# Performance work log

Measured on AMD Instinct MI355X. Metric: run time of the kernel, lower is better.

## Reference

```python
import jax, jax.numpy as jnp
import numpy as np
from jax import lax

B, CIN, COUT, WDIM, K, H, W_ = 8, 512, 512, 512, 3, 64, 64

def setup_inputs() -> dict:
    key = jax.random.key(0)
    ks = jax.random.split(key, 7)
    x = jax.random.normal(ks[0], (B, CIN, H, W_), dtype=jnp.float32)
    w = jax.random.normal(ks[1], (B, WDIM), dtype=jnp.float32)
    noise = jax.random.normal(ks[2], (B, COUT, H, W_), dtype=jnp.float32)
    # params (kaiming-ish scale for weight; demodulation normalizes anyway)
    weight = jax.random.normal(ks[3], (1, COUT, CIN, K, K), dtype=jnp.float32) * 0.05
    affine_w = jax.random.normal(ks[4], (CIN, WDIM), dtype=jnp.float32) * (1.0 / np.sqrt(WDIM))
    affine_b = jnp.zeros((CIN,), dtype=jnp.float32)
    bias = jnp.zeros((COUT,), dtype=jnp.float32)
    return {"x": x, "w": w, "noise": noise, "weight": weight,
            "affine_w": affine_w, "affine_b": affine_b, "bias": bias}

def reference(x, w, noise, weight, affine_w, affine_b, bias):
    b, cin, h, ww = x.shape
    cout, k = weight.shape[1], weight.shape[3]
    # style: affine(w) + 1
    s = jnp.einsum('bd,cd->bc', w, affine_w) + affine_b          # [B, Cin]
    s = s[:, None, :, None, None] + 1.0                           # [B,1,Cin,1,1]
    w_mod = weight * s                                            # [B,Cout,Cin,k,k]
    d = lax.rsqrt(jnp.sum(w_mod * w_mod, axis=(2, 3, 4), keepdims=True) + 1e-8)
    w_mod = w_mod * d
    # grouped conv: groups = B
    x_ = x.reshape(1, b * cin, h, ww)
    w_ = w_mod.reshape(b * cout, cin, k, k)
    pad = k // 2
    y = lax.conv_general_dilated(
        x_, w_, window_strides=(1, 1), padding=[(pad, pad), (pad, pad)],
        feature_group_count=b,
        dimension_numbers=('NCHW', 'OIHW', 'NCHW'))
    y = y.reshape(b, cout, h, ww)
    y = y + noise + bias[None, :, None, None]
    return jnp.where(y >= 0, y, 0.2 * y)
```

## Files before the change

### kernel.cpp

```cpp
#include <hip/hip_runtime.h>
#include <hip/hip_bf16.h>


#define CIN   512
#define COUT  512
#define KDIM  4608
#define HWPIX 4096

typedef __attribute__((ext_vector_type(8))) __bf16 bf16x8;
typedef __attribute__((ext_vector_type(4))) float  f32x4;

__device__ __forceinline__ unsigned short f2bf(float f){
  union { float f; unsigned int u; } v; v.f = f;
  unsigned int u = v.u;
  u += 0x7fffu + ((u >> 16) & 1u);
  return (unsigned short)(u >> 16);
}

#define GLDS16(g, l) __builtin_amdgcn_global_load_lds(                      \
    (const __attribute__((address_space(1))) unsigned int*)(g),             \
    (__attribute__((address_space(3))) unsigned int*)(l), 16, 0, 0)

__global__ void style_k(const float* __restrict__ w, const float* __restrict__ aw,
                        const float* __restrict__ ab, float* __restrict__ styles){
  int wid = threadIdx.x >> 6, lane = threadIdx.x & 63;
  int gid = blockIdx.x * 4 + wid;
  int b = gid >> 9, c = gid & 511;
  const float* wb = w + b * 512;
  const float* ar = aw + c * 512;
  float sum = 0.f;
  for (int j = lane; j < 512; j += 64) sum += wb[j] * ar[j];
  for (int off = 32; off; off >>= 1) sum += __shfl_down(sum, off, 64);
  if (lane == 0) styles[gid] = sum + ab[c] + 1.0f;
}

__global__ void modw_k(const float* __restrict__ weight, const float* __restrict__ styles,
                       unsigned short* __restrict__ wmod){
  int o = blockIdx.x, b = blockIdx.y;
  int t = threadIdx.x;
  const float* wrow = weight + (size_t)o * KDIM;
  const float* st   = styles + b * 512;
  __shared__ unsigned short sw[9 * 520];
  __shared__ float red[4];
  float vals[18];
  float part = 0.f;
#pragma unroll
  for (int it = 0; it < 18; ++it){
    int idx = it * 256 + t;
    int i = idx / 9;
    float v = wrow[idx] * st[i];
    vals[it] = v;
    part += v * v;
  }
  int wid = t >> 6, lane = t & 63;
  for (int off = 32; off; off >>= 1) part += __shfl_down(part, off, 64);
  if (lane == 0) red[wid] = part;
  __syncthreads();
  float d = rsqrtf(red[0] + red[1] + red[2] + red[3] + 1e-8f);
#pragma unroll
  for (int it = 0; it < 18; ++it){
    int idx = it * 256 + t;
    int i = idx / 9;
    int tap = idx - i * 9;
    sw[tap * 520 + i] = f2bf(vals[it] * d);
  }
  __syncthreads();
  unsigned int* orow32 = (unsigned int*)(wmod + ((size_t)(b * 512 + o)) * KDIM);
#pragma unroll
  for (int it = 0; it < 9; ++it){
    int u = it * 256 + t;
    int e = u * 2;
    int tap2 = e >> 9, i2 = e & 511;
    orow32[u] = *(const unsigned int*)&sw[tap2 * 520 + i2];
  }
}

__global__ void xpose_k(const float* __restrict__ x, unsigned short* __restrict__ xpad){
  int h = blockIdx.x, cg = blockIdx.y, b = blockIdx.z;
  int c0 = cg * 64;
  __shared__ unsigned short lds[64][66];
  int t = threadIdx.x;
  const float* xb = x + (((size_t)(b * 512 + c0)) * 64 + h) * 64;
#pragma unroll
  for (int it = 0; it < 16; ++it){
    int idx = it * 256 + t;
    int cl = idx >> 6, wl = idx & 63;
    lds[wl][cl] = f2bf(xb[(size_t)cl * 4096 + wl]);
  }
  if (t < 64){
    int which = t >> 5;
    int ch2 = (t & 31) * 2;
    int wl = which ? 65 : 0;
    *(unsigned int*)&xpad[(((size_t)b * 66 + h + 1) * 66 + wl) * 512 + c0 + ch2] = 0u;
  }
  if (h == 0 || h == 63){
    int row = (h == 0) ? 0 : 65;
    for (int u = t; u < 66 * 32; u += 256){
      int wl = u >> 5, ch2 = (u & 31) * 2;
      *(unsigned int*)&xpad[(((size_t)b * 66 + row) * 66 + wl) * 512 + c0 + ch2] = 0u;
    }
  }
  __syncthreads();
#pragma unroll
  for (int it = 0; it < 2; ++it){
    int idx = it * 256 + t;
    int wl = idx >> 3, ch = idx & 7;
    unsigned int u0 = *(const unsigned int*)&lds[wl][ch * 8 + 0];
    unsigned int u1 = *(const unsigned int*)&lds[wl][ch * 8 + 2];
    unsigned int u2 = *(const unsigned int*)&lds[wl][ch * 8 + 4];
    unsigned int u3 = *(const unsigned int*)&lds[wl][ch * 8 + 6];
    int off = ((b * 66 + h + 1) * 66 + (wl + 1)) * 512 + c0 + ch * 8;
    *(uint4*)&xpad[off] = make_uint4(u0, u1, u2, u3);
  }
}

__global__ __launch_bounds__(256, 2) void conv_gemm(
    const unsigned short* __restrict__ wmod, const unsigned short* __restrict__ xpad,
    const float* __restrict__ noise, const float* __restrict__ bias,
    float* __restrict__ out){
  __shared__ unsigned short As[2][256 * 32];
  __shared__ unsigned short Bs[2][128 * 32];
  int g = blockIdx.x;
  int xcd = g & 7, sl = g >> 3;
  int b = xcd, mt = sl >> 5, nt = sl & 31;
  int m0 = mt * 256, n0 = nt * 128;
  int h0 = nt * 2;
  int tid = threadIdx.x, wid = tid >> 6, lane = tid & 63;
  int wm = wid >> 1, wn = wid & 1;
  int lr = lane >> 2;
  int lc = lane & 3;

  const unsigned short* wbase = wmod + ((size_t)(b * 512 + m0)) * KDIM;
  int aoffG[4];
#pragma unroll
  for (int i = 0; i < 4; ++i)
    aoffG[i] = ((wid * 64 + i * 16 + lr)) * KDIM + lc * 8;

  const unsigned short* xb = xpad + (size_t)b * 66 * 66 * 512;
  int boffG[2];
#pragma unroll
  for (int i = 0; i < 2; ++i){
    int p = wid * 32 + i * 16 + lr;
    boffG[i] = ((h0 + (p >> 6) + 1) * 66 + ((p & 63) + 1)) * 512 + lc * 8;
  }
  int albase[4], blbase[2];
#pragma unroll
  for (int i = 0; i < 4; ++i) albase[i] = (wid * 64 + i * 16) * 32;
#pragma unroll
  for (int i = 0; i < 2; ++i) blbase[i] = (wid * 32 + i * 16) * 32;

  int fm = lane & 15;
  int k8 = (lane >> 4) * 8;
  int apo[8], bpo[4];
#pragma unroll
  for (int i = 0; i < 8; ++i) apo[i] = (wm * 128 + i * 16 + fm) * 32 + k8;
#pragma unroll
  for (int j = 0; j < 4; ++j) bpo[j] = (wn * 64 + j * 16 + fm) * 32 + k8;

  f32x4 acc[8][4];
#pragma unroll
  for (int i = 0; i < 8; ++i)
#pragma unroll
    for (int j = 0; j < 4; ++j) acc[i][j] = (f32x4){0.f, 0.f, 0.f, 0.f};

  for (int ks = 0; ks < 72; ++ks){
    int tap = ks >> 3;
    int c0  = (ks & 7) << 6;
    int k0  = (tap << 9) + c0;
    int dy3 = tap / 3;
    int bshift = (((dy3 - 1) * 66 + (tap - dy3 * 3 - 1)) << 9) + c0;
    __syncthreads();
#pragma unroll
    for (int i = 0; i < 4; ++i){
      GLDS16(wbase + aoffG[i] + k0,      &As[0][albase[i]]);
      GLDS16(wbase + aoffG[i] + k0 + 32, &As[1][albase[i]]);
    }
#pragma unroll
    for (int i = 0; i < 2; ++i){
      GLDS16(xb + boffG[i] + bshift,      &Bs[0][blbase[i]]);
      GLDS16(xb + boffG[i] + bshift + 32, &Bs[1][blbase[i]]);
    }
    __syncthreads();
#pragma unroll
    for (int s = 0; s < 2; ++s){
      bf16x8 af[8], bfr[4];
#pragma unroll
      for (int i = 0; i < 8; ++i) af[i]  = *(const bf16x8*)&As[s][apo[i]];
#pragma unroll
      for (int j = 0; j < 4; ++j) bfr[j] = *(const bf16x8*)&Bs[s][bpo[j]];
#pragma unroll
      for (int i = 0; i < 8; ++i)
#pragma unroll
        for (int j = 0; j < 4; ++j)
          acc[i][j] = __builtin_amdgcn_mfma_f32_16x16x32_bf16(af[i], bfr[j], acc[i][j], 0, 0, 0);
    }
  }

  int quad = lane >> 4;
#pragma unroll
  for (int i = 0; i < 8; ++i){
    int o_base = m0 + wm * 128 + i * 16 + quad * 4;
#pragma unroll
    for (int j = 0; j < 4; ++j){
      int n = n0 + wn * 64 + j * 16 + fm;
#pragma unroll
      for (int r = 0; r < 4; ++r){
        int o = o_base + r;
        size_t idx = ((size_t)(b * 512 + o)) * HWPIX + n;
        float v = acc[i][j][r] + noise[idx] + bias[o];
        out[idx] = (v >= 0.f) ? v : 0.2f * v;
      }
    }
  }
}

extern "C" void kernel_launch(void* const* d_in, const int* in_sizes, int n_in,
                              void* d_out, int out_size, void* d_ws, size_t ws_size,
                              hipStream_t stream) {
  const float* x        = (const float*)d_in[0];
  const float* w        = (const float*)d_in[1];
  const float* noise    = (const float*)d_in[2];
  const float* weight   = (const float*)d_in[3];
  const float* affine_w = (const float*)d_in[4];
  const float* affine_b = (const float*)d_in[5];
  const float* bias     = (const float*)d_in[6];
  float* out = (float*)d_out;

  float* styles = (float*)d_ws;
  unsigned short* wmod = (unsigned short*)((char*)d_ws + 16384);
  unsigned short* xpad = (unsigned short*)((char*)d_ws + 16384 + 37748736ull);

  style_k<<<dim3(1024), 256, 0, stream>>>(w, affine_w, affine_b, styles);
  modw_k <<<dim3(512, 8), 256, 0, stream>>>(weight, styles, wmod);
  xpose_k<<<dim3(64, 8, 8), 256, 0, stream>>>(x, xpad);
  conv_gemm<<<dim3(512), 256, 0, stream>>>(wmod, xpad, noise, bias, out);
}
```

Before: 336.9 us.

## Pipeline conv GEMM K-loop with triple-buffered LDS and async prefetch

Replaces the load-then-compute loop, which used two barriers per step, with a three-stage LDS ring buffer. Each stage covers 32 K elements, and loads are issued two stages ahead using direct global-to-LDS transfers. A single barrier guarded by an explicit vmcnt wait is intended to hide global load latency behind MFMA work. LDS use rises to about 72KB per block, which may limit the two-blocks-per-CU occupancy target. Correctness now depends on hand-written waitcnt counts.

```diff
diff --git a/kernel.cpp b/kernel.cpp
--- a/kernel.cpp
+++ b/kernel.cpp
@@ -114,12 +114,15 @@
   }
 }
 
+#define WAIT6 "s_waitcnt vmcnt(6) lgkmcnt(0)"
+#define WAIT0 "s_waitcnt vmcnt(0) lgkmcnt(0)"
+
 __global__ __launch_bounds__(256, 2) void conv_gemm(
     const unsigned short* __restrict__ wmod, const unsigned short* __restrict__ xpad,
     const float* __restrict__ noise, const float* __restrict__ bias,
     float* __restrict__ out){
-  __shared__ unsigned short As[2][256 * 32];
-  __shared__ unsigned short Bs[2][128 * 32];
+  __shared__ unsigned short As[3][256 * 32];
+  __shared__ unsigned short Bs[3][128 * 32];
   int g = blockIdx.x;
   int xcd = g & 7, sl = g >> 3;
   int b = xcd, mt = sl >> 5, nt = sl & 31;
@@ -163,38 +166,49 @@
 #pragma unroll
     for (int j = 0; j < 4; ++j) acc[i][j] = (f32x4){0.f, 0.f, 0.f, 0.f};
 
-  for (int ks = 0; ks < 72; ++ks){
-    int tap = ks >> 3;
-    int c0  = (ks & 7) << 6;
-    int k0  = (tap << 9) + c0;
-    int dy3 = tap / 3;
-    int bshift = (((dy3 - 1) * 66 + (tap - dy3 * 3 - 1)) << 9) + c0;
-    __syncthreads();
-#pragma unroll
-    for (int i = 0; i < 4; ++i){
-      GLDS16(wbase + aoffG[i] + k0,      &As[0][albase[i]]);
-      GLDS16(wbase + aoffG[i] + k0 + 32, &As[1][albase[i]]);
-    }
-#pragma unroll
-    for (int i = 0; i < 2; ++i){
-      GLDS16(xb + boffG[i] + bshift,      &Bs[0][blbase[i]]);
-      GLDS16(xb + boffG[i] + bshift + 32, &Bs[1][blbase[i]]);
-    }
-    __syncthreads();
-#pragma unroll
-    for (int s = 0; s < 2; ++s){
-      bf16x8 af[8], bfr[4];
-#pragma unroll
-      for (int i = 0; i < 8; ++i) af[i]  = *(const bf16x8*)&As[s][apo[i]];
-#pragma unroll
-      for (int j = 0; j < 4; ++j) bfr[j] = *(const bf16x8*)&Bs[s][bpo[j]];
-#pragma unroll
-      for (int i = 0; i < 8; ++i)
-#pragma unroll
-        for (int j = 0; j < 4; ++j)
-          acc[i][j] = __builtin_amdgcn_mfma_f32_16x16x32_bf16(af[i], bfr[j], acc[i][j], 0, 0, 0);
-    }
-  }
+#define ISSUE_STAGE(ks2, st) {                                              \
+    int tap_ = (ks2) >> 4;                                                  \
+    int c0_  = ((ks2) & 15) << 5;                                           \
+    int k0_  = (tap_ << 9) + c0_;                                           \
+    int dy3_ = tap_ / 3;                                                    \
+    int bsh_ = (((dy3_ - 1) * 66 + (tap_ - dy3_ * 3 - 1)) << 9) + c0_;      \
+    _Pragma("unroll")                                                       \
+    for (int i_ = 0; i_ < 4; ++i_)                                          \
+      GLDS16(wbase + aoffG[i_] + k0_, &As[st][albase[i_]]);                 \
+    _Pragma("unroll")                                                       \
+    for (int i_ = 0; i_ < 2; ++i_)                                          \
+      GLDS16(xb + boffG[i_] + bsh_, &Bs[st][blbase[i_]]);                   \
+  }
+
+#define COMPUTE_STAGE(st) {                                                 \
+    bf16x8 af[8], bfr[4];                                                   \
+    _Pragma("unroll")                                                       \
+    for (int i_ = 0; i_ < 8; ++i_) af[i_]  = *(const bf16x8*)&As[st][apo[i_]]; \
+    _Pragma("unroll")                                                       \
+    for (int j_ = 0; j_ < 4; ++j_) bfr[j_] = *(const bf16x8*)&Bs[st][bpo[j_]]; \
+    _Pragma("unroll")                                                       \
+    for (int i_ = 0; i_ < 8; ++i_)                                          \
+      _Pragma("unroll")                                                     \
+      for (int j_ = 0; j_ < 4; ++j_)                                        \
+        acc[i_][j_] = __builtin_amdgcn_mfma_f32_16x16x32_bf16(af[i_], bfr[j_], acc[i_][j_], 0, 0, 0); \
+  }
+
+#define BODY(ks, cst, ist, WAITSTR, DOISSUE) {                              \
+    asm volatile(WAITSTR "\n\ts_barrier" ::: "memory");                     \
+    if (DOISSUE) ISSUE_STAGE((ks) + 2, ist);                                \
+    COMPUTE_STAGE(cst);                                                     \
+  }
+
+  ISSUE_STAGE(0, 0);
+  ISSUE_STAGE(1, 1);
+  for (int kb = 0; kb < 141; kb += 3){
+    BODY(kb + 0, 0, 2, WAIT6, true);
+    BODY(kb + 1, 1, 0, WAIT6, true);
+    BODY(kb + 2, 2, 1, WAIT6, true);
+  }
+  BODY(141, 0, 2, WAIT6, true);
+  BODY(142, 1, 0, WAIT6, false);
+  BODY(143, 2, 1, WAIT0, false);
 
   int quad = lane >> 4;
 #pragma unroll
```

After: 361.8 us. 7.4% more time.
